# Kernel tuning notes

Hardware: AMD Instinct MI355X
Metric: run time of the kernel (lower is better)

Reference implementation:

```python
import jax, jax.numpy as jnp
import numpy as np

B, H, N, C = 4, 8, 2048, 32
N_SCALAR, N_VEC = 16, 4  # attn_reps = '16x0n+4x1n' -> C = 16 + 4*4 = 32
ETA = jnp.array([1.0, -1.0, -1.0, -1.0], dtype=jnp.float32)  # Minkowski metric diag


def _frame_transform(x, M):
    """Apply per-particle 4x4 matrix M to the vector channels of x.

    x: (B, H, N, C) with layout [16 scalars | 4 four-vectors]
    M: (B, N, 4, 4), shared across heads (module repeats frames over heads).
    """
    s = x[..., :N_SCALAR]                                   # (B,H,N,16) untouched
    v = x[..., N_SCALAR:].reshape(x.shape[:-1] + (N_VEC, 4))  # (B,H,N,4,4)
    v = jnp.einsum('bnij,bhnvj->bhnvi', M, v)
    return jnp.concatenate([s, v.reshape(x.shape[:-1] + (N_VEC * 4,))], axis=-1)


def setup_inputs() -> dict:
    key = jax.random.key(0)
    kq, kk, kv, kf = jax.random.split(key, 4)
    q = jax.random.normal(kq, (B, H, N, C), dtype=jnp.float32)
    k = jax.random.normal(kk, (B, H, N, C), dtype=jnp.float32)
    v = jax.random.normal(kv, (B, H, N, C), dtype=jnp.float32)
    # Genuine Lorentz frames: identity time component + random spatial rotation.
    A = jax.random.normal(kf, (B, N, 3, 3), dtype=jnp.float32)
    Q, _ = jnp.linalg.qr(A)  # (B,N,3,3) orthogonal
    frames = jnp.zeros((B, N, 4, 4), dtype=jnp.float32)
    frames = frames.at[..., 0, 0].set(1.0).at[..., 1:, 1:].set(Q)
    return {'q_local': q, 'k_local': k, 'v_local': v, 'frames': frames}


def reference(q_local, k_local, v_local, frames):
    # Inverse Lorentz frame: L^{-1} = eta L^T eta ; index-lowered inverse = L^T.
    frames_T = jnp.swapaxes(frames, -1, -2)                 # (B,N,4,4)
    inv = frames_T * ETA[:, None] * ETA[None, :]            # eta L^T eta
    lower_inv = frames_T
    # 1) local -> global frame
    q_g = _frame_transform(q_local, inv)
    k_g = _frame_transform(k_local, lower_inv)
    v_g = _frame_transform(v_local, inv)
    # 2) muP-scaled attention (1/d, not 1/sqrt(d))
    scores = jnp.einsum('bhqc,bhkc->bhqk', q_g, k_g) * (1.0 / C)
    weights = jax.nn.softmax(scores, axis=-1)
    out_g = jnp.einsum('bhqk,bhkc->bhqc', weights, v_g)
    # 3) global -> local frame
    return _frame_transform(out_g, frames)
```

## Files before the change

### kernel.cpp

```cpp
#include <hip/hip_runtime.h>
#include <hip/hip_bf16.h>


#define NB 4
#define NH 8
#define NS 2048
#define NC 32

typedef float f32x4 __attribute__((ext_vector_type(4)));
typedef short s16x8 __attribute__((ext_vector_type(8)));

#define QSCALE 0.04511260931463978f

__device__ __forceinline__ short f2bf(float f) {
  union { float f; unsigned u; } c; c.f = f;
  return (short)((c.u + 0x7FFFu + ((c.u >> 16) & 1u)) >> 16);
}

__device__ __forceinline__ void load_Q3(const float* __restrict__ F, int b, int n,
                                        float q9[9]) {
  const float* p = F + ((size_t)(b * NS + n)) * 16 + 5;
  q9[0] = p[0]; q9[1] = p[1]; q9[2] = p[2];
  q9[3] = p[4]; q9[4] = p[5]; q9[5] = p[6];
  q9[6] = p[8]; q9[7] = p[9]; q9[8] = p[10];
}

__device__ __forceinline__ void rotT(const float q9[9], f32x4& v) {
  const float x = v[1], y = v[2], z = v[3];
  v[1] = q9[0] * x + q9[3] * y + q9[6] * z;
  v[2] = q9[1] * x + q9[4] * y + q9[7] * z;
  v[3] = q9[2] * x + q9[5] * y + q9[8] * z;
}

__device__ __forceinline__ void rotF(const float q9[9], f32x4& v) {
  const float x = v[1], y = v[2], z = v[3];
  v[1] = q9[0] * x + q9[1] * y + q9[2] * z;
  v[2] = q9[3] * x + q9[4] * y + q9[5] * z;
  v[3] = q9[6] * x + q9[7] * y + q9[8] * z;
}

__launch_bounds__(256)
__global__ void rot_cast(const float* __restrict__ Qg,
                         const float* __restrict__ Kg,
                         const float* __restrict__ Vg,
                         const float* __restrict__ Fg,
                         unsigned short* __restrict__ Qbf,
                         unsigned short* __restrict__ Kbf,
                         unsigned short* __restrict__ Vbf) {
  const int gid  = blockIdx.x * 256 + threadIdx.x;
  const int tsel = gid >> 16;
  const int r    = gid & 65535;
  const int n    = r & (NS - 1);
  const int b    = r >> 14;
  const float* src = tsel == 0 ? Qg : (tsel == 1 ? Kg : Vg);
  unsigned short* dst = tsel == 0 ? Qbf : (tsel == 1 ? Kbf : Vbf);
  const float* p = src + (size_t)r * NC;
  f32x4 c[8];
#pragma unroll
  for (int i = 0; i < 8; i++) c[i] = *(const f32x4*)(p + 4 * i);
  float q9[9]; load_Q3(Fg, b, n, q9);
#pragma unroll
  for (int i = 4; i < 8; i++) rotT(q9, c[i]);
  const float s = tsel == 0 ? QSCALE : 1.0f;
  unsigned short* o = dst + (size_t)r * NC;
#pragma unroll
  for (int i = 0; i < 8; i += 2) {
    s16x8 w;
#pragma unroll
    for (int e = 0; e < 4; e++) {
      w[e]     = f2bf(c[i][e] * s);
      w[4 + e] = f2bf(c[i + 1][e] * s);
    }
    *(s16x8*)(o + 4 * i) = w;
  }
}

__launch_bounds__(256, 2)
__global__ void lloca_attn(const unsigned short* __restrict__ Qbf,
                           const unsigned short* __restrict__ Kbf,
                           const unsigned short* __restrict__ Vbf,
                           const float* __restrict__ Fg,
                           float* __restrict__ Og) {
  __shared__ __align__(16) unsigned short Klds[128 * 40];
  __shared__ __align__(16) unsigned short Vlds[32 * 136];

  const int tid  = threadIdx.x;
  const int lane = tid & 63;
  const int wv   = tid >> 6;
  const int g    = lane >> 4;
  const int lq   = lane & 15;

  const int blk = blockIdx.x;
  const int b   = blk >> 7;
  const int h   = (blk >> 4) & 7;
  const int qb  = blk & 15;

  const size_t bhr = (size_t)(b * NH + h) * NS;
  const unsigned short* Qp = Qbf + bhr * NC;
  const unsigned short* Kp = Kbf + bhr * NC;
  const unsigned short* Vp = Vbf + bhr * NC;
  float*                Op = Og  + bhr * NC;

  const int qbase = qb * 128 + wv * 32;

  const f32x4 zero4 = {0.f, 0.f, 0.f, 0.f};
  const short ONE = (short)0x3F80;
  const s16x8 ones8 = {ONE, ONE, ONE, ONE, ONE, ONE, ONE, ONE};

  s16x8 qfrag[2];
  f32x4 acc[2][2];
  f32x4 accL[2];

#pragma unroll
  for (int t = 0; t < 2; t++) {
    const int qi = qbase + t * 16 + lq;
    qfrag[t] = *(const s16x8*)(Qp + (size_t)qi * NC + g * 8);
    acc[t][0] = zero4;
    acc[t][1] = zero4;
    accL[t]   = zero4;
  }

  for (int kb = 0; kb < NS; kb += 128) {
    __syncthreads();
    {
      const int key = tid >> 1, h2 = tid & 1;
      const unsigned short* kp = Kp + (size_t)(kb + key) * NC + h2 * 16;
      s16x8 o0 = *(const s16x8*)kp;
      s16x8 o1 = *(const s16x8*)(kp + 8);
      *(s16x8*)&Klds[key * 40 + h2 * 16]     = o0;
      *(s16x8*)&Klds[key * 40 + h2 * 16 + 8] = o1;
    }
    {
      const int kp2 = tid & 63, cb = tid >> 6;
      const unsigned short* vp = Vp + (size_t)(kb + 2 * kp2) * NC + cb * 8;
      s16x8 v0 = *(const s16x8*)vp;
      s16x8 v1 = *(const s16x8*)(vp + NC);
      const int sub4   = (kp2 & 15) >> 1;
      const int newsub = (sub4 & 3) * 2 + (sub4 >> 2);
      const int pos    = (kp2 >> 4) * 32 + newsub * 4 + 2 * (kp2 & 1);
#pragma unroll
      for (int ch = 0; ch < 8; ch++) {
        unsigned uu = (unsigned)(unsigned short)v0[ch] |
                      ((unsigned)(unsigned short)v1[ch] << 16);
        *(unsigned*)&Vlds[(cb * 8 + ch) * 136 + pos] = uu;
      }
    }
    __syncthreads();

#pragma unroll
    for (int kgi = 0; kgi < 4; kgi++) {
      const int kgb = kgi * 32;
      const s16x8 kf0 = *(const s16x8*)&Klds[(kgb + lq) * 40 + g * 8];
      const s16x8 kf1 = *(const s16x8*)&Klds[(kgb + 16 + lq) * 40 + g * 8];
      const s16x8 va0 = *(const s16x8*)&Vlds[lq * 136 + kgb + g * 8];
      const s16x8 va1 = *(const s16x8*)&Vlds[(16 + lq) * 136 + kgb + g * 8];
#pragma unroll
      for (int t = 0; t < 2; t++) {
        f32x4 s0 = __builtin_amdgcn_mfma_f32_16x16x32_bf16(kf0, qfrag[t], zero4, 0, 0, 0);
        f32x4 s1 = __builtin_amdgcn_mfma_f32_16x16x32_bf16(kf1, qfrag[t], zero4, 0, 0, 0);
        float p0 = __builtin_amdgcn_exp2f(s0[0]);
        float p1 = __builtin_amdgcn_exp2f(s0[1]);
        float p2 = __builtin_amdgcn_exp2f(s0[2]);
        float p3 = __builtin_amdgcn_exp2f(s0[3]);
        float p4 = __builtin_amdgcn_exp2f(s1[0]);
        float p5 = __builtin_amdgcn_exp2f(s1[1]);
        float p6 = __builtin_amdgcn_exp2f(s1[2]);
        float p7 = __builtin_amdgcn_exp2f(s1[3]);
        union { __hip_bfloat162 h2[4]; s16x8 v; } pk;
        pk.h2[0] = __float22bfloat162_rn(make_float2(p0, p1));
        pk.h2[1] = __float22bfloat162_rn(make_float2(p2, p3));
        pk.h2[2] = __float22bfloat162_rn(make_float2(p4, p5));
        pk.h2[3] = __float22bfloat162_rn(make_float2(p6, p7));
        accL[t]   = __builtin_amdgcn_mfma_f32_16x16x32_bf16(ones8, pk.v, accL[t], 0, 0, 0);
        acc[t][0] = __builtin_amdgcn_mfma_f32_16x16x32_bf16(va0,   pk.v, acc[t][0], 0, 0, 0);
        acc[t][1] = __builtin_amdgcn_mfma_f32_16x16x32_bf16(va1,   pk.v, acc[t][1], 0, 0, 0);
      }
    }
  }

#pragma unroll
  for (int t = 0; t < 2; t++) {
    const float inv = 1.0f / accL[t][0];
    const int qi = qbase + t * 16 + lq;
    float* op = Op + (size_t)qi * NC;
    f32x4 o0, o1;
#pragma unroll
    for (int r = 0; r < 4; r++) {
      o0[r] = acc[t][0][r] * inv;
      o1[r] = acc[t][1][r] * inv;
    }
    {
      float q9[9]; load_Q3(Fg, b, qi, q9);
      rotF(q9, o1);
    }
    *(f32x4*)(op + g * 4)      = o0;
    *(f32x4*)(op + 16 + g * 4) = o1;
  }
}

extern "C" void kernel_launch(void* const* d_in, const int* in_sizes, int n_in,
                              void* d_out, int out_size, void* d_ws, size_t ws_size,
                              hipStream_t stream) {
  (void)in_sizes; (void)n_in; (void)ws_size; (void)out_size;
  const float* q = (const float*)d_in[0];
  const float* k = (const float*)d_in[1];
  const float* v = (const float*)d_in[2];
  const float* f = (const float*)d_in[3];
  float* o = (float*)d_out;

  const size_t NEL = (size_t)NB * NH * NS * NC;
  unsigned short* qbf = (unsigned short*)d_ws;
  unsigned short* kbf = qbf + NEL;
  unsigned short* vbf = kbf + NEL;

  hipLaunchKernelGGL(rot_cast, dim3(768), dim3(256), 0, stream, q, k, v, f,
                     qbf, kbf, vbf);
  hipLaunchKernelGGL(lloca_attn, dim3(512), dim3(256), 0, stream,
                     qbf, kbf, vbf, f, o);
}
```

Measured before the change: 43.94 us.

## Fuse Q rotation into attention, double-buffer K/V tiles, halve per-block query tile

Q is no longer rotated and cast by the prep kernel. The attention kernel loads fp32 Q itself, applies the frame rotation and scale, and converts it to bf16. K/V tiles are prefetched into registers and written into a second LDS buffer while the current tile is computed. Each block now handles 64 queries (one 16-query tile per wave) with a doubled grid and higher occupancy bound. This cuts prep-kernel traffic and hides global load latency, but each K/V tile is reused by fewer queries and is therefore read more often overall.

```diff
diff --git a/kernel.cpp b/kernel.cpp
--- a/kernel.cpp
+++ b/kernel.cpp
@@ -40,20 +40,18 @@
 }
 
 __launch_bounds__(256)
-__global__ void rot_cast(const float* __restrict__ Qg,
-                         const float* __restrict__ Kg,
-                         const float* __restrict__ Vg,
-                         const float* __restrict__ Fg,
-                         unsigned short* __restrict__ Qbf,
-                         unsigned short* __restrict__ Kbf,
-                         unsigned short* __restrict__ Vbf) {
+__global__ void rot_cast_kv(const float* __restrict__ Kg,
+                            const float* __restrict__ Vg,
+                            const float* __restrict__ Fg,
+                            unsigned short* __restrict__ Kbf,
+                            unsigned short* __restrict__ Vbf) {
   const int gid  = blockIdx.x * 256 + threadIdx.x;
   const int tsel = gid >> 16;
   const int r    = gid & 65535;
   const int n    = r & (NS - 1);
   const int b    = r >> 14;
-  const float* src = tsel == 0 ? Qg : (tsel == 1 ? Kg : Vg);
-  unsigned short* dst = tsel == 0 ? Qbf : (tsel == 1 ? Kbf : Vbf);
+  const float* src = tsel == 0 ? Kg : Vg;
+  unsigned short* dst = tsel == 0 ? Kbf : Vbf;
   const float* p = src + (size_t)r * NC;
   f32x4 c[8];
 #pragma unroll
@@ -61,28 +59,27 @@
   float q9[9]; load_Q3(Fg, b, n, q9);
 #pragma unroll
   for (int i = 4; i < 8; i++) rotT(q9, c[i]);
-  const float s = tsel == 0 ? QSCALE : 1.0f;
   unsigned short* o = dst + (size_t)r * NC;
 #pragma unroll
   for (int i = 0; i < 8; i += 2) {
     s16x8 w;
 #pragma unroll
     for (int e = 0; e < 4; e++) {
-      w[e]     = f2bf(c[i][e] * s);
-      w[4 + e] = f2bf(c[i + 1][e] * s);
+      w[e]     = f2bf(c[i][e]);
+      w[4 + e] = f2bf(c[i + 1][e]);
     }
     *(s16x8*)(o + 4 * i) = w;
   }
 }
 
-__launch_bounds__(256, 2)
-__global__ void lloca_attn(const unsigned short* __restrict__ Qbf,
+__launch_bounds__(256, 4)
+__global__ void lloca_attn(const float* __restrict__ Qg,
                            const unsigned short* __restrict__ Kbf,
                            const unsigned short* __restrict__ Vbf,
                            const float* __restrict__ Fg,
                            float* __restrict__ Og) {
-  __shared__ __align__(16) unsigned short Klds[128 * 40];
-  __shared__ __align__(16) unsigned short Vlds[32 * 136];
+  __shared__ __align__(16) unsigned short Klds[2][128 * 40];
+  __shared__ __align__(16) unsigned short Vlds[2][32 * 136];
 
   const int tid  = threadIdx.x;
   const int lane = tid & 63;
@@ -91,108 +88,124 @@
   const int lq   = lane & 15;
 
   const int blk = blockIdx.x;
-  const int b   = blk >> 7;
-  const int h   = (blk >> 4) & 7;
-  const int qb  = blk & 15;
+  const int b   = blk >> 8;
+  const int h   = (blk >> 5) & 7;
+  const int qb  = blk & 31;
 
   const size_t bhr = (size_t)(b * NH + h) * NS;
-  const unsigned short* Qp = Qbf + bhr * NC;
   const unsigned short* Kp = Kbf + bhr * NC;
   const unsigned short* Vp = Vbf + bhr * NC;
   float*                Op = Og  + bhr * NC;
 
-  const int qbase = qb * 128 + wv * 32;
+  const int qi = qb * 64 + wv * 16 + lq;
 
   const f32x4 zero4 = {0.f, 0.f, 0.f, 0.f};
   const short ONE = (short)0x3F80;
   const s16x8 ones8 = {ONE, ONE, ONE, ONE, ONE, ONE, ONE, ONE};
 
-  s16x8 qfrag[2];
-  f32x4 acc[2][2];
-  f32x4 accL[2];
-
-#pragma unroll
-  for (int t = 0; t < 2; t++) {
-    const int qi = qbase + t * 16 + lq;
-    qfrag[t] = *(const s16x8*)(Qp + (size_t)qi * NC + g * 8);
-    acc[t][0] = zero4;
-    acc[t][1] = zero4;
-    accL[t]   = zero4;
-  }
-
-  for (int kb = 0; kb < NS; kb += 128) {
-    __syncthreads();
-    {
-      const int key = tid >> 1, h2 = tid & 1;
-      const unsigned short* kp = Kp + (size_t)(kb + key) * NC + h2 * 16;
-      s16x8 o0 = *(const s16x8*)kp;
-      s16x8 o1 = *(const s16x8*)(kp + 8);
-      *(s16x8*)&Klds[key * 40 + h2 * 16]     = o0;
-      *(s16x8*)&Klds[key * 40 + h2 * 16 + 8] = o1;
-    }
-    {
-      const int kp2 = tid & 63, cb = tid >> 6;
-      const unsigned short* vp = Vp + (size_t)(kb + 2 * kp2) * NC + cb * 8;
-      s16x8 v0 = *(const s16x8*)vp;
-      s16x8 v1 = *(const s16x8*)(vp + NC);
-      const int sub4   = (kp2 & 15) >> 1;
-      const int newsub = (sub4 & 3) * 2 + (sub4 >> 2);
-      const int pos    = (kp2 >> 4) * 32 + newsub * 4 + 2 * (kp2 & 1);
-#pragma unroll
-      for (int ch = 0; ch < 8; ch++) {
-        unsigned uu = (unsigned)(unsigned short)v0[ch] |
-                      ((unsigned)(unsigned short)v1[ch] << 16);
-        *(unsigned*)&Vlds[(cb * 8 + ch) * 136 + pos] = uu;
-      }
-    }
-    __syncthreads();
-
+  s16x8 qfrag;
+  {
+    const float* qp = Qg + (bhr + qi) * NC + g * 8;
+    f32x4 a = *(const f32x4*)qp;
+    f32x4 c = *(const f32x4*)(qp + 4);
+    if (g >= 2) {
+      float q9[9]; load_Q3(Fg, b, qi, q9);
+      rotT(q9, a);
+      rotT(q9, c);
+    }
+#pragma unroll
+    for (int e = 0; e < 4; e++) {
+      qfrag[e]     = f2bf(a[e] * QSCALE);
+      qfrag[4 + e] = f2bf(c[e] * QSCALE);
+    }
+  }
+
+  f32x4 acc0 = zero4, acc1 = zero4, accL = zero4;
+
+  const int key = tid >> 1, h2 = tid & 1;
+  const int kp2 = tid & 63, cb = tid >> 6;
+  const int sub4   = (kp2 & 15) >> 1;
+  const int newsub = (sub4 & 3) * 2 + (sub4 >> 2);
+  const int vpos   = (kp2 >> 4) * 32 + newsub * 4 + 2 * (kp2 & 1);
+  const unsigned short* kbase = Kp + (size_t)key * NC + h2 * 16;
+  const unsigned short* vbase = Vp + (size_t)(2 * kp2) * NC + cb * 8;
+
+  s16x8 rk0, rk1, rv0, rv1;
+
+  rk0 = *(const s16x8*)kbase;
+  rk1 = *(const s16x8*)(kbase + 8);
+  rv0 = *(const s16x8*)vbase;
+  rv1 = *(const s16x8*)(vbase + NC);
+
+#define WRITE_TILE(buf)                                                        \
+  do {                                                                         \
+    *(s16x8*)&Klds[buf][key * 40 + h2 * 16]     = rk0;                         \
+    *(s16x8*)&Klds[buf][key * 40 + h2 * 16 + 8] = rk1;                         \
+    _Pragma("unroll")                                                          \
+    for (int ch = 0; ch < 8; ch++) {                                           \
+      unsigned uu = (unsigned)(unsigned short)rv0[ch] |                        \
+                    ((unsigned)(unsigned short)rv1[ch] << 16);                 \
+      *(unsigned*)&Vlds[buf][(cb * 8 + ch) * 136 + vpos] = uu;                 \
+    }                                                                          \
+  } while (0)
+
+  WRITE_TILE(0);
+  __syncthreads();
+
+  const int NT = NS / 128;
+  for (int i = 0; i < NT; i++) {
+    const int cur = i & 1;
+    if (i + 1 < NT) {
+      const size_t off = (size_t)(i + 1) * 128 * NC;
+      rk0 = *(const s16x8*)(kbase + off);
+      rk1 = *(const s16x8*)(kbase + off + 8);
+      rv0 = *(const s16x8*)(vbase + off);
+      rv1 = *(const s16x8*)(vbase + off + NC);
+    }
 #pragma unroll
     for (int kgi = 0; kgi < 4; kgi++) {
       const int kgb = kgi * 32;
-      const s16x8 kf0 = *(const s16x8*)&Klds[(kgb + lq) * 40 + g * 8];
-      const s16x8 kf1 = *(const s16x8*)&Klds[(kgb + 16 + lq) * 40 + g * 8];
-      const s16x8 va0 = *(const s16x8*)&Vlds[lq * 136 + kgb + g * 8];
-      const s16x8 va1 = *(const s16x8*)&Vlds[(16 + lq) * 136 + kgb + g * 8];
-#pragma unroll
-      for (int t = 0; t < 2; t++) {
-        f32x4 s0 = __builtin_amdgcn_mfma_f32_16x16x32_bf16(kf0, qfrag[t], zero4, 0, 0, 0);
-        f32x4 s1 = __builtin_amdgcn_mfma_f32_16x16x32_bf16(kf1, qfrag[t], zero4, 0, 0, 0);
-        float p0 = __builtin_amdgcn_exp2f(s0[0]);
-        float p1 = __builtin_amdgcn_exp2f(s0[1]);
-        float p2 = __builtin_amdgcn_exp2f(s0[2]);
-        float p3 = __builtin_amdgcn_exp2f(s0[3]);
-        float p4 = __builtin_amdgcn_exp2f(s1[0]);
-        float p5 = __builtin_amdgcn_exp2f(s1[1]);
-        float p6 = __builtin_amdgcn_exp2f(s1[2]);
-        float p7 = __builtin_amdgcn_exp2f(s1[3]);
-        union { __hip_bfloat162 h2[4]; s16x8 v; } pk;
-        pk.h2[0] = __float22bfloat162_rn(make_float2(p0, p1));
-        pk.h2[1] = __float22bfloat162_rn(make_float2(p2, p3));
-        pk.h2[2] = __float22bfloat162_rn(make_float2(p4, p5));
-        pk.h2[3] = __float22bfloat162_rn(make_float2(p6, p7));
-        accL[t]   = __builtin_amdgcn_mfma_f32_16x16x32_bf16(ones8, pk.v, accL[t], 0, 0, 0);
-        acc[t][0] = __builtin_amdgcn_mfma_f32_16x16x32_bf16(va0,   pk.v, acc[t][0], 0, 0, 0);
-        acc[t][1] = __builtin_amdgcn_mfma_f32_16x16x32_bf16(va1,   pk.v, acc[t][1], 0, 0, 0);
-      }
-    }
-  }
-
-#pragma unroll
-  for (int t = 0; t < 2; t++) {
-    const float inv = 1.0f / accL[t][0];
-    const int qi = qbase + t * 16 + lq;
+      const s16x8 kf0 = *(const s16x8*)&Klds[cur][(kgb + lq) * 40 + g * 8];
+      const s16x8 kf1 = *(const s16x8*)&Klds[cur][(kgb + 16 + lq) * 40 + g * 8];
+      const s16x8 va0 = *(const s16x8*)&Vlds[cur][lq * 136 + kgb + g * 8];
+      const s16x8 va1 = *(const s16x8*)&Vlds[cur][(16 + lq) * 136 + kgb + g * 8];
+      f32x4 s0 = __builtin_amdgcn_mfma_f32_16x16x32_bf16(kf0, qfrag, zero4, 0, 0, 0);
+      f32x4 s1 = __builtin_amdgcn_mfma_f32_16x16x32_bf16(kf1, qfrag, zero4, 0, 0, 0);
+      float p0 = __builtin_amdgcn_exp2f(s0[0]);
+      float p1 = __builtin_amdgcn_exp2f(s0[1]);
+      float p2 = __builtin_amdgcn_exp2f(s0[2]);
+      float p3 = __builtin_amdgcn_exp2f(s0[3]);
+      float p4 = __builtin_amdgcn_exp2f(s1[0]);
+      float p5 = __builtin_amdgcn_exp2f(s1[1]);
+      float p6 = __builtin_amdgcn_exp2f(s1[2]);
+      float p7 = __builtin_amdgcn_exp2f(s1[3]);
+      union { __hip_bfloat162 h2[4]; s16x8 v; } pk;
+      pk.h2[0] = __float22bfloat162_rn(make_float2(p0, p1));
+      pk.h2[1] = __float22bfloat162_rn(make_float2(p2, p3));
+      pk.h2[2] = __float22bfloat162_rn(make_float2(p4, p5));
+      pk.h2[3] = __float22bfloat162_rn(make_float2(p6, p7));
+      accL = __builtin_amdgcn_mfma_f32_16x16x32_bf16(ones8, pk.v, accL, 0, 0, 0);
+      acc0 = __builtin_amdgcn_mfma_f32_16x16x32_bf16(va0,   pk.v, acc0, 0, 0, 0);
+      acc1 = __builtin_amdgcn_mfma_f32_16x16x32_bf16(va1,   pk.v, acc1, 0, 0, 0);
+    }
+    __syncthreads();
+    if (i + 1 < NT) {
+      WRITE_TILE(cur ^ 1);
+      __syncthreads();
+    }
+  }
+
+  {
+    const float inv = 1.0f / accL[0];
     float* op = Op + (size_t)qi * NC;
     f32x4 o0, o1;
 #pragma unroll
     for (int r = 0; r < 4; r++) {
-      o0[r] = acc[t][0][r] * inv;
-      o1[r] = acc[t][1][r] * inv;
-    }
-    {
-      float q9[9]; load_Q3(Fg, b, qi, q9);
-      rotF(q9, o1);
-    }
+      o0[r] = acc0[r] * inv;
+      o1[r] = acc1[r] * inv;
+    }
+    float q9[9]; load_Q3(Fg, b, qi, q9);
+    rotF(q9, o1);
     *(f32x4*)(op + g * 4)      = o0;
     *(f32x4*)(op + 16 + g * 4) = o1;
   }
@@ -209,12 +222,11 @@
   float* o = (float*)d_out;
 
   const size_t NEL = (size_t)NB * NH * NS * NC;
-  unsigned short* qbf = (unsigned short*)d_ws;
-  unsigned short* kbf = qbf + NEL;
+  unsigned short* kbf = (unsigned short*)d_ws;
   unsigned short* vbf = kbf + NEL;
 
-  hipLaunchKernelGGL(rot_cast, dim3(768), dim3(256), 0, stream, q, k, v, f,
-                     qbf, kbf, vbf);
-  hipLaunchKernelGGL(lloca_attn, dim3(512), dim3(256), 0, stream,
-                     qbf, kbf, vbf, f, o);
-}
+  hipLaunchKernelGGL(rot_cast_kv, dim3(512), dim3(256), 0, stream,
+                     k, v, f, kbf, vbf);
+  hipLaunchKernelGGL(lloca_attn, dim3(1024), dim3(256), 0, stream,
+                     q, kbf, vbf, f, o);
+}
```

Measured after the change: 44.54 us. About the same (+1.4%).
